# Optimization experiments

Hardware: AMD Instinct MI355X
Metric: run time of the kernel (lower is better)

The kernel has to match this reference:

```python
import jax, jax.numpy as jnp
import numpy as np
from jax import lax

B, IC, OC = 1, 16, 32
K, STRIDE, PAD, DIL = 3, 1, 1, 1
D = 32  # each of the 4 spatial dims


def setup_inputs() -> dict:
    key = jax.random.key(0)
    k1, k2, k3 = jax.random.split(key, 3)
    inputs = jax.random.normal(k1, (B, IC, D, D, D, D), dtype=jnp.float32)
    weight = jax.random.normal(k2, (OC, IC * K ** 4), dtype=jnp.float32)
    bias = jax.random.normal(k3, (1, OC, 1, 1, 1, 1), dtype=jnp.float32)
    return {"inputs": inputs, "weight": weight, "bias": bias}


def _conv4d(x, w_flat):
    # x: [B, IC, D1, D2, D3, D4]; w_flat: [OC, IC*K^4]
    b, c, d1, d2, d3, d4 = x.shape
    w = w_flat.reshape(OC, c, K, K, K, K)
    o1 = (d1 + 2 * PAD - DIL * (K - 1) - 1) // STRIDE + 1
    # pad only the first spatial dim; 3D conv handles the rest
    xp = jnp.pad(x, ((0, 0), (0, 0), (PAD, PAD), (0, 0), (0, 0), (0, 0)))
    out = None
    for ki in range(K):  # small fixed loop over first kernel dim
        start = ki * DIL
        xs = lax.slice_in_dim(xp, start, start + (o1 - 1) * STRIDE + 1, stride=STRIDE, axis=2)
        # [B, C, O1, D2, D3, D4] -> fold O1 into batch for a 3D conv
        xb = xs.transpose(0, 2, 1, 3, 4, 5).reshape(b * o1, c, d2, d3, d4)
        y = lax.conv_general_dilated(
            xb, w[:, :, ki],
            window_strides=(STRIDE,) * 3,
            padding=[(PAD, PAD)] * 3,
            rhs_dilation=(DIL,) * 3,
            dimension_numbers=("NCDHW", "OIDHW", "NCDHW"))
        out = y if out is None else out + y
    _, _, o2, o3, o4 = out.shape
    out = out.reshape(b, o1, OC, o2, o3, o4).transpose(0, 2, 1, 3, 4, 5)
    return out  # [B, OC, O1, O2, O3, O4]


def reference(inputs, weight, bias):
    return _conv4d(inputs, weight) + bias
```

## Files before the change

kernel.cpp:

```cpp
#include <hip/hip_runtime.h>
#include <hip/hip_bf16.h>
#include <stdint.h>


typedef __bf16 bf16x8 __attribute__((ext_vector_type(8)));
typedef float f32x16 __attribute__((ext_vector_type(16)));

#define X_IC_STRIDE 1048576
#define W_K 1296
#define WPACK_DWORDS 23040
#define XPACK_OFF 98304
#define XPACK_BYTES 33554432u
#define ZOFF XPACK_BYTES
#define LDS_BYTES (13 * 256 * 16)

__device__ __forceinline__ unsigned rne_bf16(float f) {
    unsigned b = __builtin_bit_cast(unsigned, f);
    return (b + 0x7FFFu + ((b >> 16) & 1u)) >> 16;
}

__device__ __forceinline__ void gload_lds16(const unsigned char* g, unsigned char* s) {
    __builtin_amdgcn_global_load_lds(
        (const __attribute__((address_space(1))) unsigned int*)g,
        (__attribute__((address_space(3))) unsigned int*)s, 16, 0, 0);
}

__global__ void pack_w_kernel(const float* __restrict__ w, unsigned* __restrict__ wpack) {
    int D = blockIdx.x * 256 + threadIdx.x;
    if (D >= WPACK_DWORDS) return;
    int t    = D & 3;
    int lane = (D >> 2) & 63;
    int fi   = D >> 8;
    int p    = fi % 5;
    int dadb = (fi / 5) % 9;
    int g    = fi / 45;
    int kh   = lane >> 5;
    int oc   = lane & 31;
    int slot = 2 * p + kh;
    unsigned pk = 0u;
    if (slot < 9) {
        int da = dadb / 3, db = dadb % 3;
        int dc = slot / 3, dd = slot % 3;
        int koff = da * 27 + db * 9 + dc * 3 + dd;
        int ic0  = g * 8 + 2 * t;
        unsigned lo = rne_bf16(w[oc * W_K + ic0 * 81 + koff]);
        unsigned hi = rne_bf16(w[oc * W_K + (ic0 + 1) * 81 + koff]);
        pk = lo | (hi << 16);
    }
    wpack[D] = pk;
}

__global__ __launch_bounds__(256) void pack_x_kernel(const float* __restrict__ x,
                                                     unsigned char* __restrict__ xpack) {
    unsigned P0 = (blockIdx.x * 256 + threadIdx.x) * 4;
    float4 v[16];
#pragma unroll
    for (int ic = 0; ic < 16; ++ic)
        v[ic] = *(const float4*)(x + (size_t)ic * X_IC_STRIDE + P0);
    uint4 o[8];
#pragma unroll
    for (int pt = 0; pt < 4; ++pt) {
        unsigned u[16];
#pragma unroll
        for (int ic = 0; ic < 16; ++ic) {
            float f = (pt == 0) ? v[ic].x : (pt == 1) ? v[ic].y
                    : (pt == 2) ? v[ic].z : v[ic].w;
            u[ic] = rne_bf16(f);
        }
        o[pt * 2]     = make_uint4(u[0] | (u[1] << 16),  u[2] | (u[3] << 16),
                                   u[4] | (u[5] << 16),  u[6] | (u[7] << 16));
        o[pt * 2 + 1] = make_uint4(u[8] | (u[9] << 16),  u[10] | (u[11] << 16),
                                   u[12] | (u[13] << 16), u[14] | (u[15] << 16));
    }
#pragma unroll
    for (int j = 0; j < 8; ++j)
        *(uint4*)(xpack + (size_t)P0 * 32 + j * 16) = o[j];
    if (P0 == 0) {
        *(uint4*)(xpack + ZOFF) = make_uint4(0u, 0u, 0u, 0u);
        *(uint4*)(xpack + ZOFF + 16) = make_uint4(0u, 0u, 0u, 0u);
    }
}

template <int XP>
__global__ __launch_bounds__(256, 3) void conv4d_mfma(
    const float* __restrict__ x,
    const unsigned char* __restrict__ wpack,
    const unsigned char* __restrict__ xpack,
    const float* __restrict__ bias,
    float* __restrict__ out)
{
    __shared__ __attribute__((aligned(16))) unsigned char lds[LDS_BYTES];

    const int tid  = threadIdx.x;
    const int lane = tid & 63;
    const int wv   = tid >> 6;
    const int kh   = lane >> 5;
    const int ln   = lane & 31;

    const int bid = blockIdx.x;
    const int blk = ((bid & 7) << 8) | (bid >> 3);
    const int c0  = (blk & 7) * 4;
    const int b0  = ((blk >> 3) & 15) * 2;
    const int a0  = (blk >> 7) * 2;
    const int ai  = wv >> 1, bi = wv & 1;

    int pbase[3];
#pragma unroll
    for (int p = 0; p < 3; ++p) {
        int slot = 2 * p + kh;
        int dc = slot / 3, dd = slot % 3;
        pbase[p] = dc * 544 + (ln + dd) * 16;
    }

    unsigned xoff[13];
    if (XP) {
#pragma unroll
        for (int it = 0; it < 13; ++it) {
            int t   = tid + it * 256;
            int dpr = t % 34;
            int row = t / 34;
            int rc = row % 6; int r2 = row / 6;
            int rb = r2 & 3;  int ra = r2 >> 2;
            int a_in = a0 + ra - 1, b_in = b0 + rb - 1;
            int c_in = c0 + rc - 1, d_in = dpr - 1;
            bool v = ((unsigned)a_in < 32u) & ((unsigned)b_in < 32u) &
                     ((unsigned)c_in < 32u) & ((unsigned)d_in < 32u);
            unsigned P = (unsigned)(((a_in * 32 + b_in) * 32 + c_in) * 32 + d_in);
            xoff[it] = v ? P * 32u : ZOFF;
        }
    }

    f32x16 acc[4];
#pragma unroll
    for (int ci = 0; ci < 4; ++ci)
#pragma unroll
        for (int r = 0; r < 16; ++r) acc[ci][r] = 0.f;

    bf16x8 af[5];
#pragma unroll
    for (int p = 0; p < 5; ++p)
        af[p] = *(const bf16x8*)(wpack + (size_t)p * 1024 + lane * 16);

    for (int g = 0; g < 2; ++g) {
        if (g) __syncthreads();
        if (XP) {
            const int gofs = g << 4;
#pragma unroll
            for (int it = 0; it < 13; ++it)
                gload_lds16(xpack + xoff[it] + gofs,
                            lds + ((it * 256 + (wv << 6)) << 4));
        } else {
            for (int t = tid; t < 96 * 34; t += 256) {
                int dpr = t % 34;
                int row = t / 34;
                int rc = row % 6; int r2 = row / 6;
                int rb = r2 & 3;  int ra = r2 >> 2;
                int a_in = a0 + ra - 1, b_in = b0 + rb - 1;
                int c_in = c0 + rc - 1, d_in = dpr - 1;
                uint4 pk = make_uint4(0u, 0u, 0u, 0u);
                if ((unsigned)a_in < 32u && (unsigned)b_in < 32u &&
                    (unsigned)c_in < 32u && (unsigned)d_in < 32u) {
                    const float* xp = x + (size_t)(g * 8) * X_IC_STRIDE +
                                      (((a_in * 32 + b_in) * 32 + c_in) * 32 + d_in);
                    unsigned u[8];
#pragma unroll
                    for (int j = 0; j < 8; ++j)
                        u[j] = rne_bf16(xp[j * X_IC_STRIDE]);
                    pk.x = u[0] | (u[1] << 16); pk.y = u[2] | (u[3] << 16);
                    pk.z = u[4] | (u[5] << 16); pk.w = u[6] | (u[7] << 16);
                }
                *(uint4*)(lds + t * 16) = pk;
            }
        }
        __syncthreads();

        for (int dadb = 0; dadb < 9; ++dadb) {
            const int fi  = g * 9 + dadb;
            const int nfi = (fi + 1 > 17) ? 17 : fi + 1;
            bf16x8 afn[5];
#pragma unroll
            for (int p = 0; p < 5; ++p)
                afn[p] = *(const bf16x8*)(wpack + ((size_t)nfi * 5 + p) * 1024 + lane * 16);

            const int da = dadb / 3, db = dadb % 3;
            const int ubase = ((ai + da) * 24 + (bi + db) * 6) * 544;

            __builtin_amdgcn_s_setprio(1);
#pragma unroll
            for (int p = 0; p < 2; ++p) {
                const unsigned char* bp = lds + ubase + pbase[p];
                bf16x8 f6[6];
#pragma unroll
                for (int j = 0; j < 6; ++j)
                    f6[j] = *(const bf16x8*)(bp + j * 544);
#pragma unroll
                for (int ci = 0; ci < 4; ++ci)
                    acc[ci] = __builtin_amdgcn_mfma_f32_32x32x16_bf16(
                        af[p], f6[ci], acc[ci], 0, 0, 0);
#pragma unroll
                for (int ci = 0; ci < 4; ++ci)
                    acc[ci] = __builtin_amdgcn_mfma_f32_32x32x16_bf16(
                        af[p + 3], f6[ci + 2], acc[ci], 0, 0, 0);
            }
            {
                const unsigned char* bp = lds + ubase + pbase[2];
#pragma unroll
                for (int ci = 0; ci < 4; ++ci) {
                    bf16x8 bfrag = *(const bf16x8*)(bp + ci * 544);
                    acc[ci] = __builtin_amdgcn_mfma_f32_32x32x16_bf16(
                        af[2], bfrag, acc[ci], 0, 0, 0);
                }
            }
            __builtin_amdgcn_s_setprio(0);
#pragma unroll
            for (int p = 0; p < 5; ++p) af[p] = afn[p];
        }
    }

    float bv[16];
#pragma unroll
    for (int r = 0; r < 16; ++r) bv[r] = bias[(r & 3) + 8 * (r >> 2) + 4 * kh];

    const size_t sp_base = (((size_t)(a0 + ai) * 32 + (b0 + bi)) * 32 + c0);
#pragma unroll
    for (int ci = 0; ci < 4; ++ci) {
#pragma unroll
        for (int r = 0; r < 16; ++r) {
            int oc_ = (r & 3) + 8 * (r >> 2) + 4 * kh;
            out[(size_t)oc_ * X_IC_STRIDE + (sp_base + ci) * 32 + ln] = acc[ci][r] + bv[r];
        }
    }
}

extern "C" void kernel_launch(void* const* d_in, const int* in_sizes, int n_in,
                              void* d_out, int out_size, void* d_ws, size_t ws_size,
                              hipStream_t stream) {
    const float* x    = (const float*)d_in[0];
    const float* w    = (const float*)d_in[1];
    const float* bias = (const float*)d_in[2];
    float* out        = (float*)d_out;
    unsigned* wpack   = (unsigned*)d_ws;
    unsigned char* xpack = (unsigned char*)d_ws + XPACK_OFF;

    pack_w_kernel<<<dim3((WPACK_DWORDS + 255) / 256), dim3(256), 0, stream>>>(w, wpack);
    if (ws_size >= (size_t)XPACK_OFF + XPACK_BYTES + 32) {
        pack_x_kernel<<<dim3(1024), dim3(256), 0, stream>>>(x, xpack);
        conv4d_mfma<1><<<dim3(2048), dim3(256), 0, stream>>>(
            x, (const unsigned char*)d_ws, xpack, bias, out);
    } else {
        conv4d_mfma<0><<<dim3(2048), dim3(256), 0, stream>>>(
            x, (const unsigned char*)d_ws, xpack, bias, out);
    }
}
```

Baseline: 279.3 us.

## Split LDS staging into halves to overlap channel-group loads with MFMA

Divides the 52KB LDS tile into two halves along the first spatial dimension and splits the staging loop into per-half stages. The second channel group's loads are issued into each half as soon as the first group's compute on that half is finished. Meanwhile MFMA work continues on the other half, so the global-to-LDS load latency is meant to hide behind compute instead of stalling at a full barrier. The cost is more complex staging logic, extra offset registers and more barriers. The fallback path is moved into a separate legacy kernel.

```diff
diff --git a/kernel.cpp b/kernel.cpp
--- a/kernel.cpp
+++ b/kernel.cpp
@@ -12,7 +12,9 @@
 #define XPACK_OFF 98304
 #define XPACK_BYTES 33554432u
 #define ZOFF XPACK_BYTES
-#define LDS_BYTES (13 * 256 * 16)
+#define H_SLOTS 1632
+#define H_BYTES 26624
+#define LEGACY_LDS 52224
 
 __device__ __forceinline__ unsigned rne_bf16(float f) {
     unsigned b = __builtin_bit_cast(unsigned, f);
@@ -24,6 +26,8 @@
         (const __attribute__((address_space(1))) unsigned int*)g,
         (__attribute__((address_space(3))) unsigned int*)s, 16, 0, 0);
 }
+
+__device__ __forceinline__ void fence_sched() { __builtin_amdgcn_sched_barrier(0); }
 
 __global__ void pack_w_kernel(const float* __restrict__ w, unsigned* __restrict__ wpack) {
     int D = blockIdx.x * 256 + threadIdx.x;
@@ -81,15 +85,14 @@
     }
 }
 
-template <int XP>
-__global__ __launch_bounds__(256, 3) void conv4d_mfma(
-    const float* __restrict__ x,
+__global__ __launch_bounds__(256, 3) void conv4d_pipe(
     const unsigned char* __restrict__ wpack,
     const unsigned char* __restrict__ xpack,
     const float* __restrict__ bias,
     float* __restrict__ out)
 {
-    __shared__ __attribute__((aligned(16))) unsigned char lds[LDS_BYTES];
+    __shared__ __attribute__((aligned(16))) unsigned char ldsH0[H_BYTES];
+    __shared__ __attribute__((aligned(16))) unsigned char ldsH1[H_BYTES];
 
     const int tid  = threadIdx.x;
     const int lane = tid & 63;
@@ -112,65 +115,194 @@
         pbase[p] = dc * 544 + (ln + dd) * 16;
     }
 
-    unsigned xoff[13];
-    if (XP) {
-#pragma unroll
-        for (int it = 0; it < 13; ++it) {
-            int t   = tid + it * 256;
+    const int nld   = (wv < 2) ? 7 : 6;
+    const int sbase = (wv < 2) ? wv * 448 : 896 + (wv - 2) * 384;
+
+    unsigned xoffH[2][7];
+#pragma unroll
+    for (int h = 0; h < 2; ++h)
+#pragma unroll
+        for (int i = 0; i < 7; ++i) {
+            int s   = sbase + i * 64 + lane;
+            int row = h * 48 + s / 34;
+            int dpr = s % 34;
+            int rc = row % 6; int r2 = row / 6;
+            int rb = r2 & 3;  int ra = r2 >> 2;
+            int a_in = a0 + ra - 1, b_in = b0 + rb - 1;
+            int c_in = c0 + rc - 1, d_in = dpr - 1;
+            bool v = (s < H_SLOTS) &
+                     ((unsigned)a_in < 32u) & ((unsigned)b_in < 32u) &
+                     ((unsigned)c_in < 32u) & ((unsigned)d_in < 32u);
+            unsigned P = (unsigned)(((a_in * 32 + b_in) * 32 + c_in) * 32 + d_in);
+            xoffH[h][i] = v ? P * 32u : ZOFF;
+        }
+
+    f32x16 acc[4];
+#pragma unroll
+    for (int ci = 0; ci < 4; ++ci)
+#pragma unroll
+        for (int r = 0; r < 16; ++r) acc[ci][r] = 0.f;
+
+    bf16x8 af[5];
+
+    auto stage_half = [&](unsigned char* dstArr, int h, int g) {
+        const unsigned gofs = (unsigned)(g << 4);
+        unsigned char* base = dstArr + (sbase << 4);
+#pragma unroll
+        for (int i = 0; i < 7; ++i) {
+            if (i < 6 || wv < 2) {
+                if (i < nld)
+                    gload_lds16(xpack + xoffH[h][i] + gofs, base + ((i * 64) << 4));
+            }
+        }
+    };
+
+    auto cstep = [&](int g, int da) {
+        const int ca = ai + da;
+        const unsigned char* hb = ((ca & 2) ? ldsH1 : ldsH0) + (ca & 1) * 13056;
+#pragma unroll
+        for (int db = 0; db < 3; ++db) {
+            const int fi  = g * 9 + da * 3 + db;
+            const int nfi = (fi + 1 > 17) ? 17 : fi + 1;
+            bf16x8 afn[5];
+#pragma unroll
+            for (int p = 0; p < 5; ++p)
+                afn[p] = *(const bf16x8*)(wpack + ((size_t)nfi * 5 + p) * 1024 + lane * 16);
+
+            const unsigned char* rbase = hb + (bi + db) * 3264;
+            __builtin_amdgcn_s_setprio(1);
+#pragma unroll
+            for (int p = 0; p < 2; ++p) {
+                const unsigned char* bp = rbase + pbase[p];
+                bf16x8 f6[6];
+#pragma unroll
+                for (int j = 0; j < 6; ++j)
+                    f6[j] = *(const bf16x8*)(bp + j * 544);
+#pragma unroll
+                for (int ci = 0; ci < 4; ++ci)
+                    acc[ci] = __builtin_amdgcn_mfma_f32_32x32x16_bf16(
+                        af[p], f6[ci], acc[ci], 0, 0, 0);
+#pragma unroll
+                for (int ci = 0; ci < 4; ++ci)
+                    acc[ci] = __builtin_amdgcn_mfma_f32_32x32x16_bf16(
+                        af[p + 3], f6[ci + 2], acc[ci], 0, 0, 0);
+            }
+            {
+                const unsigned char* bp = rbase + pbase[2];
+#pragma unroll
+                for (int ci = 0; ci < 4; ++ci) {
+                    bf16x8 bfrag = *(const bf16x8*)(bp + ci * 544);
+                    acc[ci] = __builtin_amdgcn_mfma_f32_32x32x16_bf16(
+                        af[2], bfrag, acc[ci], 0, 0, 0);
+                }
+            }
+            __builtin_amdgcn_s_setprio(0);
+#pragma unroll
+            for (int p = 0; p < 5; ++p) af[p] = afn[p];
+        }
+    };
+
+    stage_half(ldsH0, 0, 0);
+    stage_half(ldsH1, 1, 0);
+#pragma unroll
+    for (int p = 0; p < 5; ++p)
+        af[p] = *(const bf16x8*)(wpack + (size_t)p * 1024 + lane * 16);
+    __syncthreads();
+
+    cstep(0, 0);
+    cstep(0, 1);
+    __syncthreads();
+
+    stage_half(ldsH0, 0, 1);
+    fence_sched();
+    cstep(0, 2);
+    __syncthreads();
+
+    stage_half(ldsH1, 1, 1);
+    fence_sched();
+    cstep(1, 0);
+    __syncthreads();
+
+    cstep(1, 1);
+    cstep(1, 2);
+
+    float bv[16];
+#pragma unroll
+    for (int r = 0; r < 16; ++r) bv[r] = bias[(r & 3) + 8 * (r >> 2) + 4 * kh];
+
+    const size_t sp_base = (((size_t)(a0 + ai) * 32 + (b0 + bi)) * 32 + c0);
+#pragma unroll
+    for (int ci = 0; ci < 4; ++ci) {
+#pragma unroll
+        for (int r = 0; r < 16; ++r) {
+            int oc_ = (r & 3) + 8 * (r >> 2) + 4 * kh;
+            out[(size_t)oc_ * X_IC_STRIDE + (sp_base + ci) * 32 + ln] = acc[ci][r] + bv[r];
+        }
+    }
+}
+
+__global__ __launch_bounds__(256, 3) void conv4d_legacy(
+    const float* __restrict__ x,
+    const unsigned char* __restrict__ wpack,
+    const float* __restrict__ bias,
+    float* __restrict__ out)
+{
+    __shared__ __attribute__((aligned(16))) unsigned char lds[LEGACY_LDS];
+
+    const int tid  = threadIdx.x;
+    const int lane = tid & 63;
+    const int wv   = tid >> 6;
+    const int kh   = lane >> 5;
+    const int ln   = lane & 31;
+
+    const int bid = blockIdx.x;
+    const int blk = ((bid & 7) << 8) | (bid >> 3);
+    const int c0  = (blk & 7) * 4;
+    const int b0  = ((blk >> 3) & 15) * 2;
+    const int a0  = (blk >> 7) * 2;
+    const int ai  = wv >> 1, bi = wv & 1;
+
+    int pbase[3];
+#pragma unroll
+    for (int p = 0; p < 3; ++p) {
+        int slot = 2 * p + kh;
+        int dc = slot / 3, dd = slot % 3;
+        pbase[p] = dc * 544 + (ln + dd) * 16;
+    }
+
+    f32x16 acc[4];
+#pragma unroll
+    for (int ci = 0; ci < 4; ++ci)
+#pragma unroll
+        for (int r = 0; r < 16; ++r) acc[ci][r] = 0.f;
+
+    bf16x8 af[5];
+#pragma unroll
+    for (int p = 0; p < 5; ++p)
+        af[p] = *(const bf16x8*)(wpack + (size_t)p * 1024 + lane * 16);
+
+    for (int g = 0; g < 2; ++g) {
+        if (g) __syncthreads();
+        for (int t = tid; t < 96 * 34; t += 256) {
             int dpr = t % 34;
             int row = t / 34;
             int rc = row % 6; int r2 = row / 6;
             int rb = r2 & 3;  int ra = r2 >> 2;
             int a_in = a0 + ra - 1, b_in = b0 + rb - 1;
             int c_in = c0 + rc - 1, d_in = dpr - 1;
-            bool v = ((unsigned)a_in < 32u) & ((unsigned)b_in < 32u) &
-                     ((unsigned)c_in < 32u) & ((unsigned)d_in < 32u);
-            unsigned P = (unsigned)(((a_in * 32 + b_in) * 32 + c_in) * 32 + d_in);
-            xoff[it] = v ? P * 32u : ZOFF;
-        }
-    }
-
-    f32x16 acc[4];
-#pragma unroll
-    for (int ci = 0; ci < 4; ++ci)
-#pragma unroll
-        for (int r = 0; r < 16; ++r) acc[ci][r] = 0.f;
-
-    bf16x8 af[5];
-#pragma unroll
-    for (int p = 0; p < 5; ++p)
-        af[p] = *(const bf16x8*)(wpack + (size_t)p * 1024 + lane * 16);
-
-    for (int g = 0; g < 2; ++g) {
-        if (g) __syncthreads();
-        if (XP) {
-            const int gofs = g << 4;
-#pragma unroll
-            for (int it = 0; it < 13; ++it)
-                gload_lds16(xpack + xoff[it] + gofs,
-                            lds + ((it * 256 + (wv << 6)) << 4));
-        } else {
-            for (int t = tid; t < 96 * 34; t += 256) {
-                int dpr = t % 34;
-                int row = t / 34;
-                int rc = row % 6; int r2 = row / 6;
-                int rb = r2 & 3;  int ra = r2 >> 2;
-                int a_in = a0 + ra - 1, b_in = b0 + rb - 1;
-                int c_in = c0 + rc - 1, d_in = dpr - 1;
-                uint4 pk = make_uint4(0u, 0u, 0u, 0u);
-                if ((unsigned)a_in < 32u && (unsigned)b_in < 32u &&
-                    (unsigned)c_in < 32u && (unsigned)d_in < 32u) {
-                    const float* xp = x + (size_t)(g * 8) * X_IC_STRIDE +
-                                      (((a_in * 32 + b_in) * 32 + c_in) * 32 + d_in);
-                    unsigned u[8];
-#pragma unroll
-                    for (int j = 0; j < 8; ++j)
-                        u[j] = rne_bf16(xp[j * X_IC_STRIDE]);
-                    pk.x = u[0] | (u[1] << 16); pk.y = u[2] | (u[3] << 16);
-                    pk.z = u[4] | (u[5] << 16); pk.w = u[6] | (u[7] << 16);
-                }
-                *(uint4*)(lds + t * 16) = pk;
-            }
+            uint4 pk = make_uint4(0u, 0u, 0u, 0u);
+            if ((unsigned)a_in < 32u && (unsigned)b_in < 32u &&
+                (unsigned)c_in < 32u && (unsigned)d_in < 32u) {
+                const float* xp = x + (size_t)(g * 8) * X_IC_STRIDE +
+                                  (((a_in * 32 + b_in) * 32 + c_in) * 32 + d_in);
+                unsigned u[8];
+#pragma unroll
+                for (int j = 0; j < 8; ++j)
+                    u[j] = rne_bf16(xp[j * X_IC_STRIDE]);
+                pk.x = u[0] | (u[1] << 16); pk.y = u[2] | (u[3] << 16);
+                pk.z = u[4] | (u[5] << 16); pk.w = u[6] | (u[7] << 16);
+            }
+            *(uint4*)(lds + t * 16) = pk;
         }
         __syncthreads();
 
@@ -184,8 +316,6 @@
 
             const int da = dadb / 3, db = dadb % 3;
             const int ubase = ((ai + da) * 24 + (bi + db) * 6) * 544;
-
-            __builtin_amdgcn_s_setprio(1);
 #pragma unroll
             for (int p = 0; p < 2; ++p) {
                 const unsigned char* bp = lds + ubase + pbase[p];
@@ -211,7 +341,6 @@
                         af[2], bfrag, acc[ci], 0, 0, 0);
                 }
             }
-            __builtin_amdgcn_s_setprio(0);
 #pragma unroll
             for (int p = 0; p < 5; ++p) af[p] = afn[p];
         }
@@ -245,10 +374,10 @@
     pack_w_kernel<<<dim3((WPACK_DWORDS + 255) / 256), dim3(256), 0, stream>>>(w, wpack);
     if (ws_size >= (size_t)XPACK_OFF + XPACK_BYTES + 32) {
         pack_x_kernel<<<dim3(1024), dim3(256), 0, stream>>>(x, xpack);
-        conv4d_mfma<1><<<dim3(2048), dim3(256), 0, stream>>>(
-            x, (const unsigned char*)d_ws, xpack, bias, out);
+        conv4d_pipe<<<dim3(2048), dim3(256), 0, stream>>>(
+            (const unsigned char*)d_ws, xpack, bias, out);
     } else {
-        conv4d_mfma<0><<<dim3(2048), dim3(256), 0, stream>>>(
-            x, (const unsigned char*)d_ws, xpack, bias, out);
-    }
-}
+        conv4d_legacy<<<dim3(2048), dim3(256), 0, stream>>>(
+            x, (const unsigned char*)d_ws, bias, out);
+    }
+}
```

Result: no change. 275.5 us (-1.4%).
